# Performance work log

Measured on AMD Instinct MI355X. Metric: run time of the kernel, lower is better.

The kernel has to match this reference:

```python
import jax, jax.numpy as jnp
import numpy as np

B, C, H, W = 4, 256, 64, 64
CI = C // 2
EPS = 1e-5


def setup_inputs() -> dict:
    key = jax.random.key(0)
    ks = jax.random.split(key, 3)
    return {
        "x": jax.random.normal(ks[0], (B, C, H, W), dtype=jnp.float32) * 0.1,
        "g_w": jax.random.normal(ks[1], (CI, C), dtype=jnp.float32) * 0.05,
        "g_b": jnp.zeros((CI,), dtype=jnp.float32),
        "W_w": jax.random.normal(ks[2], (C, CI), dtype=jnp.float32) * 0.05,
        "W_b": jnp.zeros((C,), dtype=jnp.float32),
        "gamma": jnp.ones((C,), dtype=jnp.float32),
        "beta": jnp.zeros((C,), dtype=jnp.float32),
    }


def reference(x, g_w, g_b, W_w, W_b, gamma, beta):
    b, c, h, w = x.shape
    n = h * w
    ci = g_w.shape[0]
    # g: 1x1 conv C -> C/2
    g_x = jnp.einsum('oc,bchw->bohw', g_w, x) + g_b[None, :, None, None]
    g_x = g_x.reshape(b, ci, n).transpose(0, 2, 1)          # [B, N, Ci]
    theta = x.reshape(b, c, n).transpose(0, 2, 1)           # [B, N, C]
    phi = x.reshape(b, c, n)                                # [B, C, N]
    f = jnp.einsum('bnc,bcm->bnm', theta, phi)              # [B, N, N]
    attn = jax.nn.softmax(f, axis=-1)
    y = jnp.einsum('bnm,bmc->bnc', attn, g_x)               # [B, N, Ci]
    y = y.transpose(0, 2, 1).reshape(b, ci, h, w)
    # W: 1x1 conv C/2 -> C, then BatchNorm2d (training-mode batch stats)
    wy = jnp.einsum('oc,bchw->bohw', W_w, y) + W_b[None, :, None, None]
    mean = wy.mean(axis=(0, 2, 3))
    var = wy.var(axis=(0, 2, 3))  # biased, as torch BN uses for normalization
    wy = (wy - mean[None, :, None, None]) * jax.lax.rsqrt(var[None, :, None, None] + EPS)
    wy = wy * gamma[None, :, None, None] + beta[None, :, None, None]
    return wy + x
```

## Files before the change

kernel.cpp:

```cpp
#include <hip/hip_runtime.h>
#include <math.h>

#define B_ 4
#define C_ 256
#define CI_ 128
#define N_ 4096
#define QT_ 128
#define KT_ 64
#define KH_ 2048
#define NITER (KH_ / KT_)
#define KSTRIDE 264
#define VSTRIDE 72
constexpr float EPS_ = 1e-5f;

typedef __attribute__((ext_vector_type(8))) short bfrag;
typedef __attribute__((ext_vector_type(4))) float f4;

__device__ __forceinline__ unsigned short bf16r(float x) {
    unsigned u = __float_as_uint(x);
    u += 0x7FFFu + ((u >> 16) & 1u);
    return (unsigned short)(u >> 16);
}
__device__ __forceinline__ unsigned pack_bf16(float a, float b) {
    unsigned ua = __float_as_uint(a); ua += 0x7FFFu + ((ua >> 16) & 1u);
    unsigned ub = __float_as_uint(b); ub += 0x7FFFu + ((ub >> 16) & 1u);
    return (ua >> 16) | (ub & 0xFFFF0000u);
}

__global__ __launch_bounds__(256) void make_xt(const float* __restrict__ x,
                                               unsigned short* __restrict__ xt,
                                               float* __restrict__ sums) {
    if (blockIdx.x == 0 && blockIdx.y == 0 && blockIdx.z == 0) {
        sums[threadIdx.x] = 0.f;
        sums[threadIdx.x + 256] = 0.f;
    }
    int n  = blockIdx.x * 256 + threadIdx.x;
    int c0 = blockIdx.y * 8;
    int b  = blockIdx.z;
    const float* xb = x + (size_t)b * C_ * N_;
    unsigned short buf[8];
#pragma unroll
    for (int c = 0; c < 8; c++) buf[c] = bf16r(xb[(c0 + c) * N_ + n]);
    uint4 v;
    v.x = buf[0] | ((unsigned)buf[1] << 16);
    v.y = buf[2] | ((unsigned)buf[3] << 16);
    v.z = buf[4] | ((unsigned)buf[5] << 16);
    v.w = buf[6] | ((unsigned)buf[7] << 16);
    *(uint4*)&xt[((size_t)b * N_ + n) * C_ + c0] = v;
}

__global__ __launch_bounds__(256) void gconv(const float* __restrict__ x,
                                             const float* __restrict__ gw,
                                             const float* __restrict__ gb,
                                             unsigned short* __restrict__ gx) {
    int m  = blockIdx.x * 256 + threadIdx.x;
    int o0 = blockIdx.y * 16;
    int b  = blockIdx.z;
    const float* xb = x + (size_t)b * C_ * N_;
    float acc[16];
#pragma unroll
    for (int o = 0; o < 16; o++) acc[o] = gb[o0 + o];
    for (int c0 = 0; c0 < C_; c0 += 8) {
        float xv[8];
#pragma unroll
        for (int j = 0; j < 8; j++) xv[j] = xb[(c0 + j) * N_ + m];
#pragma unroll
        for (int o = 0; o < 16; o++) {
            const float* wr = gw + (size_t)(o0 + o) * C_ + c0;
#pragma unroll
            for (int j = 0; j < 8; j++) acc[o] += wr[j] * xv[j];
        }
    }
#pragma unroll
    for (int o = 0; o < 16; o++)
        gx[((size_t)b * CI_ + o0 + o) * N_ + m] = bf16r(acc[o]);
}

__global__ __launch_bounds__(1024, 4) void attn(const unsigned short* __restrict__ xt,
                                                const unsigned short* __restrict__ gx,
                                                float* __restrict__ Yp,
                                                float* __restrict__ ml) {
    __shared__ __align__(16) unsigned short Ks[2][64 * KSTRIDE];
    __shared__ __align__(16) unsigned short Vs[2][128 * VSTRIDE];
    __shared__ __align__(16) unsigned short Ps[128 * VSTRIDE];

    const int tid  = threadIdx.x;
    const int lane = tid & 63, w = tid >> 6;
    const int wq = w & 7, g = w >> 3;
    const int quad = lane >> 4, ql = lane & 15;
    const int half = blockIdx.x & 1;
    const int b    = (blockIdx.x & 7) >> 1;
    const int qt   = blockIdx.x >> 3;
    const int n0   = qt * QT_;
    const int kbase = half * KH_;
    const unsigned short* xtb = xt + (size_t)b * N_ * C_;
    const unsigned short* gxb = gx + (size_t)b * CI_ * N_;

    bfrag qb[8];
#pragma unroll
    for (int ks = 0; ks < 8; ks++)
        qb[ks] = *(const bfrag*)(xtb + (size_t)(n0 + 16 * wq + ql) * C_ + 32 * ks + quad * 8);

    f4 yacc[8];
    const f4 zero4 = {0.f, 0.f, 0.f, 0.f};
#pragma unroll
    for (int i = 0; i < 8; i++) yacc[i] = zero4;
    float mrun = -INFINITY, lrun = 0.f;

    uint4 kreg[2], vreg[1];
#pragma unroll
    for (int r = 0; r < 2; r++) {
        int idx = r * 1024 + tid;
        kreg[r] = *(const uint4*)(xtb + (size_t)(kbase + (idx >> 5)) * C_ + (idx & 31) * 8);
    }
    vreg[0] = *(const uint4*)(gxb + (size_t)(tid >> 3) * N_ + kbase + (tid & 7) * 8);
#pragma unroll
    for (int r = 0; r < 2; r++) {
        int idx = r * 1024 + tid;
        *(uint4*)&Ks[0][(idx >> 5) * KSTRIDE + (idx & 31) * 8] = kreg[r];
    }
    *(uint4*)&Vs[0][(tid >> 3) * VSTRIDE + (tid & 7) * 8] = vreg[0];
#pragma unroll
    for (int r = 0; r < 2; r++) {
        int idx = r * 1024 + tid;
        kreg[r] = *(const uint4*)(xtb + (size_t)(kbase + KT_ + (idx >> 5)) * C_ + (idx & 31) * 8);
    }
    vreg[0] = *(const uint4*)(gxb + (size_t)(tid >> 3) * N_ + kbase + KT_ + (tid & 7) * 8);
    __syncthreads();

    for (int it = 0; it < NITER; ++it) {
        const int cur = it & 1, nxt = cur ^ 1;

        if (it + 1 < NITER) {
#pragma unroll
            for (int r = 0; r < 2; r++) {
                int idx = r * 1024 + tid;
                *(uint4*)&Ks[nxt][(idx >> 5) * KSTRIDE + (idx & 31) * 8] = kreg[r];
            }
            *(uint4*)&Vs[nxt][(tid >> 3) * VSTRIDE + (tid & 7) * 8] = vreg[0];
        }
        if (it + 2 < NITER) {
            const int t0 = kbase + (it + 2) * KT_;
#pragma unroll
            for (int r = 0; r < 2; r++) {
                int idx = r * 1024 + tid;
                kreg[r] = *(const uint4*)(xtb + (size_t)(t0 + (idx >> 5)) * C_ + (idx & 31) * 8);
            }
            vreg[0] = *(const uint4*)(gxb + (size_t)(tid >> 3) * N_ + t0 + (tid & 7) * 8);
        }

        f4 sacc[2];
        sacc[0] = zero4; sacc[1] = zero4;
#pragma unroll
        for (int ks = 0; ks < 8; ks++) {
            bfrag ka[2];
#pragma unroll
            for (int i = 0; i < 2; i++)
                ka[i] = *(const bfrag*)&Ks[cur][(32 * g + 16 * i + ql) * KSTRIDE + 32 * ks + quad * 8];
#pragma unroll
            for (int i = 0; i < 2; i++)
                sacc[i] = __builtin_amdgcn_mfma_f32_16x16x32_bf16(ka[i], qb[ks], sacc[i], 0, 0, 0);
        }

        float mx = -INFINITY;
#pragma unroll
        for (int i = 0; i < 2; i++)
#pragma unroll
            for (int r = 0; r < 4; r++) mx = fmaxf(mx, sacc[i][r]);
        mx = fmaxf(mx, __shfl_xor(mx, 16, 64));
        mx = fmaxf(mx, __shfl_xor(mx, 32, 64));
        float mn = fmaxf(mrun, mx);
        float alpha = __expf(mrun - mn);
        mrun = mn;
        lrun *= alpha;
        if (__any(alpha != 1.f)) {
#pragma unroll
            for (int i = 0; i < 8; i++) {
                yacc[i][0] *= alpha; yacc[i][1] *= alpha;
                yacc[i][2] *= alpha; yacc[i][3] *= alpha;
            }
        }

        {
            int q = 16 * wq + ql;
            float lsum = 0.f;
#pragma unroll
            for (int i = 0; i < 2; i++) {
                float p0 = __expf(sacc[i][0] - mrun);
                float p1 = __expf(sacc[i][1] - mrun);
                float p2 = __expf(sacc[i][2] - mrun);
                float p3 = __expf(sacc[i][3] - mrun);
                lsum += (p0 + p1) + (p2 + p3);
                int idx = q * VSTRIDE + 32 * g + 16 * i + 4 * quad;
                unsigned long long pv = (unsigned long long)pack_bf16(p0, p1)
                                      | ((unsigned long long)pack_bf16(p2, p3) << 32);
                *(unsigned long long*)&Ps[idx] = pv;
            }
            lrun += lsum;
        }

        {
            bfrag pb, va[8];
            pb = *(const bfrag*)&Ps[(16 * wq + ql) * VSTRIDE + 32 * g + quad * 8];
#pragma unroll
            for (int i = 0; i < 8; i++)
                va[i] = *(const bfrag*)&Vs[cur][(16 * i + ql) * VSTRIDE + 32 * g + quad * 8];
#pragma unroll
            for (int i = 0; i < 8; i++)
                yacc[i] = __builtin_amdgcn_mfma_f32_16x16x32_bf16(va[i], pb, yacc[i], 0, 0, 0);
        }

        __syncthreads();
    }

    lrun += __shfl_xor(lrun, 16, 64);
    lrun += __shfl_xor(lrun, 32, 64);

    float* PsF = (float*)Ps;
    float* Ysc = PsF;
    float* mlb = PsF + 4096;

    const int q = 16 * wq + ql;
    if (quad == 0) {
        mlb[(g * 128 + q) * 2]     = mrun;
        mlb[(g * 128 + q) * 2 + 1] = lrun;
    }
    __syncthreads();
    float m0 = mlb[q * 2],           l0 = mlb[q * 2 + 1];
    float m1 = mlb[(128 + q) * 2],   l1 = mlb[(128 + q) * 2 + 1];
    float mm = fmaxf(m0, m1);
    float e0 = __expf(m0 - mm), e1 = __expf(m1 - mm);
    float lnew = e0 * l0 + e1 * l1;

#pragma unroll
    for (int c = 0; c < 4; c++) {
        if (g == 1) {
#pragma unroll
            for (int i2 = 0; i2 < 2; i2++) {
                int i = 2 * c + i2;
#pragma unroll
                for (int r = 0; r < 4; r++) {
                    int cip = 16 * i2 + 4 * quad + r;
                    Ysc[cip * 128 + q] = e1 * yacc[i][r];
                }
            }
        }
        __syncthreads();
        if (g == 0) {
#pragma unroll
            for (int i2 = 0; i2 < 2; i2++) {
                int i = 2 * c + i2;
#pragma unroll
                for (int r = 0; r < 4; r++) {
                    int ci = 16 * i + 4 * quad + r;
                    float v = e0 * yacc[i][r] + Ysc[(16 * i2 + 4 * quad + r) * 128 + q];
                    Yp[(((size_t)half * 4 + b) * CI_ + ci) * N_ + n0 + q] = v;
                }
            }
        }
        __syncthreads();
    }
    if (g == 0 && quad == 0) {
        ml[(((size_t)half * 4 + b) * N_ + n0 + q) * 2]     = mm;
        ml[(((size_t)half * 4 + b) * N_ + n0 + q) * 2 + 1] = lnew;
    }
}

__global__ __launch_bounds__(256) void merge(const float* __restrict__ Yp,
                                             const float* __restrict__ ml,
                                             float* __restrict__ y) {
    int n4 = blockIdx.x * 256 + threadIdx.x;
    int ci = blockIdx.y;
    int b  = blockIdx.z;
    int n  = n4 * 4;
    float4 a0 = *(const float4*)&ml[((size_t)b * N_ + n) * 2];
    float4 a1 = *(const float4*)&ml[((size_t)b * N_ + n + 2) * 2];
    float4 c0 = *(const float4*)&ml[(((size_t)4 + b) * N_ + n) * 2];
    float4 c1 = *(const float4*)&ml[(((size_t)4 + b) * N_ + n + 2) * 2];
    float m0[4] = {a0.x, a0.z, a1.x, a1.z};
    float l0[4] = {a0.y, a0.w, a1.y, a1.w};
    float m1[4] = {c0.x, c0.z, c1.x, c1.z};
    float l1[4] = {c0.y, c0.w, c1.y, c1.w};
    float w0[4], w1[4];
#pragma unroll
    for (int k = 0; k < 4; k++) {
        float mm = fmaxf(m0[k], m1[k]);
        float e0 = __expf(m0[k] - mm), e1 = __expf(m1[k] - mm);
        float inv = 1.f / (e0 * l0[k] + e1 * l1[k]);
        w0[k] = e0 * inv;
        w1[k] = e1 * inv;
    }
    size_t base = ((size_t)b * CI_ + ci) * N_ + n;
    float4 y0 = *(const float4*)&Yp[base];
    float4 y1 = *(const float4*)&Yp[(size_t)4 * CI_ * N_ + base];
    float4 o;
    o.x = w0[0] * y0.x + w1[0] * y1.x;
    o.y = w0[1] * y0.y + w1[1] * y1.y;
    o.z = w0[2] * y0.z + w1[2] * y1.z;
    o.w = w0[3] * y0.w + w1[3] * y1.w;
    *(float4*)&y[base] = o;
}

__global__ __launch_bounds__(256) void wconv_stats(const float* __restrict__ y,
                                                   const float* __restrict__ Ww,
                                                   const float* __restrict__ Wb,
                                                   float* __restrict__ wy,
                                                   float* __restrict__ sums) {
    int n   = blockIdx.x * 256 + threadIdx.x;
    int co0 = blockIdx.y * 16;
    int b   = blockIdx.z;
    const float* yb = y + (size_t)b * CI_ * N_;
    float acc[16];
#pragma unroll
    for (int o = 0; o < 16; o++) acc[o] = Wb[co0 + o];
    for (int c0 = 0; c0 < CI_; c0 += 8) {
        float yv[8];
#pragma unroll
        for (int j = 0; j < 8; j++) yv[j] = yb[(c0 + j) * N_ + n];
#pragma unroll
        for (int o = 0; o < 16; o++) {
            const float* wr = Ww + (size_t)(co0 + o) * CI_ + c0;
#pragma unroll
            for (int j = 0; j < 8; j++) acc[o] += wr[j] * yv[j];
        }
    }
    float* wyb = wy + (size_t)b * C_ * N_;
#pragma unroll
    for (int o = 0; o < 16; o++) wyb[(co0 + o) * N_ + n] = acc[o];

    __shared__ float wred[32][4];
    int lane = threadIdx.x & 63, wid = threadIdx.x >> 6;
#pragma unroll
    for (int o = 0; o < 16; o++) {
        float s1 = acc[o], s2 = acc[o] * acc[o];
#pragma unroll
        for (int off = 32; off > 0; off >>= 1) {
            s1 += __shfl_down(s1, off, 64);
            s2 += __shfl_down(s2, off, 64);
        }
        if (lane == 0) { wred[o][wid] = s1; wred[16 + o][wid] = s2; }
    }
    __syncthreads();
    if (threadIdx.x < 32) {
        int qq = threadIdx.x;
        float t = wred[qq][0] + wred[qq][1] + wred[qq][2] + wred[qq][3];
        int o = qq & 15;
        if (qq < 16) atomicAdd(&sums[co0 + o], t);
        else         atomicAdd(&sums[256 + co0 + o], t);
    }
}

__global__ __launch_bounds__(256) void bn_finalize(float* __restrict__ wy,
                                                   const float* __restrict__ x,
                                                   const float* __restrict__ sums,
                                                   const float* __restrict__ gamma,
                                                   const float* __restrict__ beta,
                                                   float* __restrict__ out) {
    int n4 = blockIdx.x * 256 + threadIdx.x;
    int co = blockIdx.y;
    int b  = blockIdx.z;
    float cnt  = (float)(B_ * N_);
    float mean = sums[co] / cnt;
    float var  = sums[256 + co] / cnt - mean * mean;
    float sc   = rsqrtf(var + EPS_) * gamma[co];
    float bt   = beta[co];
    size_t idx = ((size_t)b * C_ + co) * N_ + (size_t)n4 * 4;
    float4 wv = *(const float4*)&wy[idx];
    float4 xv = *(const float4*)&x[idx];
    float4 o;
    o.x = (wv.x - mean) * sc + bt + xv.x;
    o.y = (wv.y - mean) * sc + bt + xv.y;
    o.z = (wv.z - mean) * sc + bt + xv.z;
    o.w = (wv.w - mean) * sc + bt + xv.w;
    *(float4*)&out[idx] = o;
}

extern "C" void kernel_launch(void* const* d_in, const int* in_sizes, int n_in,
                              void* d_out, int out_size, void* d_ws, size_t ws_size,
                              hipStream_t stream) {
    const float* x     = (const float*)d_in[0];
    const float* gw    = (const float*)d_in[1];
    const float* gb    = (const float*)d_in[2];
    const float* Ww    = (const float*)d_in[3];
    const float* Wb    = (const float*)d_in[4];
    const float* gamma = (const float*)d_in[5];
    const float* beta  = (const float*)d_in[6];
    float* out = (float*)d_out;
    float* ws  = (float*)d_ws;

    unsigned short* xt  = (unsigned short*)ws;
    unsigned short* gxb = (unsigned short*)(ws + 2097152);
    float* Yp   = ws + 3145728;
    float* ml   = ws + 7340032;
    float* sums = ws + 7405568;
    float* y    = ws;
    float* wy   = out;

    hipLaunchKernelGGL(make_xt, dim3(16, 32, 4), dim3(256), 0, stream, x, xt, sums);
    hipLaunchKernelGGL(gconv, dim3(16, 8, 4), dim3(256), 0, stream, x, gw, gb, gxb);
    hipLaunchKernelGGL(attn, dim3(256), dim3(1024), 0, stream, xt, gxb, Yp, ml);
    hipLaunchKernelGGL(merge, dim3(4, 128, 4), dim3(256), 0, stream, Yp, ml, y);
    hipLaunchKernelGGL(wconv_stats, dim3(16, 16, 4), dim3(256), 0, stream, y, Ww, Wb, wy, sums);
    hipLaunchKernelGGL(bn_finalize, dim3(4, 256, 4), dim3(256), 0, stream, wy, x, sums, gamma, beta, out);
}
```

Measured before the change: 283.5 us.

## Switch attention kernel to 32x32x16 MFMA tiles with 512-thread blocks

Reworks the attention kernel to use 32x32x16 bf16 MFMA instead of 16x16x32, with 8 waves per block (4 query groups by 2 key halves) instead of 16. Each wave now owns a 32-query by 32-key tile, so it issues fewer, larger MFMAs and reuses each LDS fragment load across more arithmetic. Two independent score accumulators are summed to shorten the dependency chain. The cost is higher register pressure per thread (16 Q fragments and four 16-wide accumulators) and fewer waves per block available to hide latency.

```diff
diff --git a/kernel.cpp b/kernel.cpp
--- a/kernel.cpp
+++ b/kernel.cpp
@@ -15,6 +15,7 @@
 
 typedef __attribute__((ext_vector_type(8))) short bfrag;
 typedef __attribute__((ext_vector_type(4))) float f4;
+typedef __attribute__((ext_vector_type(16))) float facc16;
 
 __device__ __forceinline__ unsigned short bf16r(float x) {
     unsigned u = __float_as_uint(x);
@@ -76,18 +77,18 @@
         gx[((size_t)b * CI_ + o0 + o) * N_ + m] = bf16r(acc[o]);
 }
 
-__global__ __launch_bounds__(1024, 4) void attn(const unsigned short* __restrict__ xt,
-                                                const unsigned short* __restrict__ gx,
-                                                float* __restrict__ Yp,
-                                                float* __restrict__ ml) {
+__global__ __launch_bounds__(512, 2) void attn(const unsigned short* __restrict__ xt,
+                                               const unsigned short* __restrict__ gx,
+                                               float* __restrict__ Yp,
+                                               float* __restrict__ ml) {
     __shared__ __align__(16) unsigned short Ks[2][64 * KSTRIDE];
     __shared__ __align__(16) unsigned short Vs[2][128 * VSTRIDE];
     __shared__ __align__(16) unsigned short Ps[128 * VSTRIDE];
 
     const int tid  = threadIdx.x;
     const int lane = tid & 63, w = tid >> 6;
-    const int wq = w & 7, g = w >> 3;
-    const int quad = lane >> 4, ql = lane & 15;
+    const int wq = w & 3, g = w >> 2;
+    const int col = lane & 31, h = lane >> 5;
     const int half = blockIdx.x & 1;
     const int b    = (blockIdx.x & 7) >> 1;
     const int qt   = blockIdx.x >> 3;
@@ -96,36 +97,49 @@
     const unsigned short* xtb = xt + (size_t)b * N_ * C_;
     const unsigned short* gxb = gx + (size_t)b * CI_ * N_;
 
-    bfrag qb[8];
-#pragma unroll
-    for (int ks = 0; ks < 8; ks++)
-        qb[ks] = *(const bfrag*)(xtb + (size_t)(n0 + 16 * wq + ql) * C_ + 32 * ks + quad * 8);
-
-    f4 yacc[8];
-    const f4 zero4 = {0.f, 0.f, 0.f, 0.f};
-#pragma unroll
-    for (int i = 0; i < 8; i++) yacc[i] = zero4;
+    bfrag qb[16];
+#pragma unroll
+    for (int kc = 0; kc < 16; kc++)
+        qb[kc] = *(const bfrag*)(xtb + (size_t)(n0 + 32 * wq + col) * C_ + kc * 16 + h * 8);
+
+    facc16 yacc[4];
+#pragma unroll
+    for (int t = 0; t < 4; t++)
+#pragma unroll
+        for (int r = 0; r < 16; r++) yacc[t][r] = 0.f;
     float mrun = -INFINITY, lrun = 0.f;
 
-    uint4 kreg[2], vreg[1];
+    uint4 kreg[4], vreg[2];
+#pragma unroll
+    for (int r = 0; r < 4; r++) {
+        int idx = r * 512 + tid;
+        kreg[r] = *(const uint4*)(xtb + (size_t)(kbase + (idx >> 5)) * C_ + (idx & 31) * 8);
+    }
 #pragma unroll
     for (int r = 0; r < 2; r++) {
-        int idx = r * 1024 + tid;
-        kreg[r] = *(const uint4*)(xtb + (size_t)(kbase + (idx >> 5)) * C_ + (idx & 31) * 8);
-    }
-    vreg[0] = *(const uint4*)(gxb + (size_t)(tid >> 3) * N_ + kbase + (tid & 7) * 8);
+        int idx = r * 512 + tid;
+        vreg[r] = *(const uint4*)(gxb + (size_t)(idx >> 3) * N_ + kbase + (idx & 7) * 8);
+    }
+#pragma unroll
+    for (int r = 0; r < 4; r++) {
+        int idx = r * 512 + tid;
+        *(uint4*)&Ks[0][(idx >> 5) * KSTRIDE + (idx & 31) * 8] = kreg[r];
+    }
 #pragma unroll
     for (int r = 0; r < 2; r++) {
-        int idx = r * 1024 + tid;
-        *(uint4*)&Ks[0][(idx >> 5) * KSTRIDE + (idx & 31) * 8] = kreg[r];
-    }
-    *(uint4*)&Vs[0][(tid >> 3) * VSTRIDE + (tid & 7) * 8] = vreg[0];
+        int idx = r * 512 + tid;
+        *(uint4*)&Vs[0][(idx >> 3) * VSTRIDE + (idx & 7) * 8] = vreg[r];
+    }
+#pragma unroll
+    for (int r = 0; r < 4; r++) {
+        int idx = r * 512 + tid;
+        kreg[r] = *(const uint4*)(xtb + (size_t)(kbase + KT_ + (idx >> 5)) * C_ + (idx & 31) * 8);
+    }
 #pragma unroll
     for (int r = 0; r < 2; r++) {
-        int idx = r * 1024 + tid;
-        kreg[r] = *(const uint4*)(xtb + (size_t)(kbase + KT_ + (idx >> 5)) * C_ + (idx & 31) * 8);
-    }
-    vreg[0] = *(const uint4*)(gxb + (size_t)(tid >> 3) * N_ + kbase + KT_ + (tid & 7) * 8);
+        int idx = r * 512 + tid;
+        vreg[r] = *(const uint4*)(gxb + (size_t)(idx >> 3) * N_ + kbase + KT_ + (idx & 7) * 8);
+    }
     __syncthreads();
 
     for (int it = 0; it < NITER; ++it) {
@@ -133,41 +147,45 @@
 
         if (it + 1 < NITER) {
 #pragma unroll
+            for (int r = 0; r < 4; r++) {
+                int idx = r * 512 + tid;
+                *(uint4*)&Ks[nxt][(idx >> 5) * KSTRIDE + (idx & 31) * 8] = kreg[r];
+            }
+#pragma unroll
             for (int r = 0; r < 2; r++) {
-                int idx = r * 1024 + tid;
-                *(uint4*)&Ks[nxt][(idx >> 5) * KSTRIDE + (idx & 31) * 8] = kreg[r];
-            }
-            *(uint4*)&Vs[nxt][(tid >> 3) * VSTRIDE + (tid & 7) * 8] = vreg[0];
+                int idx = r * 512 + tid;
+                *(uint4*)&Vs[nxt][(idx >> 3) * VSTRIDE + (idx & 7) * 8] = vreg[r];
+            }
         }
         if (it + 2 < NITER) {
             const int t0 = kbase + (it + 2) * KT_;
 #pragma unroll
+            for (int r = 0; r < 4; r++) {
+                int idx = r * 512 + tid;
+                kreg[r] = *(const uint4*)(xtb + (size_t)(t0 + (idx >> 5)) * C_ + (idx & 31) * 8);
+            }
+#pragma unroll
             for (int r = 0; r < 2; r++) {
-                int idx = r * 1024 + tid;
-                kreg[r] = *(const uint4*)(xtb + (size_t)(t0 + (idx >> 5)) * C_ + (idx & 31) * 8);
-            }
-            vreg[0] = *(const uint4*)(gxb + (size_t)(tid >> 3) * N_ + t0 + (tid & 7) * 8);
-        }
-
-        f4 sacc[2];
-        sacc[0] = zero4; sacc[1] = zero4;
-#pragma unroll
-        for (int ks = 0; ks < 8; ks++) {
-            bfrag ka[2];
-#pragma unroll
-            for (int i = 0; i < 2; i++)
-                ka[i] = *(const bfrag*)&Ks[cur][(32 * g + 16 * i + ql) * KSTRIDE + 32 * ks + quad * 8];
-#pragma unroll
-            for (int i = 0; i < 2; i++)
-                sacc[i] = __builtin_amdgcn_mfma_f32_16x16x32_bf16(ka[i], qb[ks], sacc[i], 0, 0, 0);
-        }
+                int idx = r * 512 + tid;
+                vreg[r] = *(const uint4*)(gxb + (size_t)(idx >> 3) * N_ + t0 + (idx & 7) * 8);
+            }
+        }
+
+        facc16 sa, sb;
+#pragma unroll
+        for (int r = 0; r < 16; r++) { sa[r] = 0.f; sb[r] = 0.f; }
+#pragma unroll
+        for (int kc = 0; kc < 8; kc++) {
+            bfrag ka0 = *(const bfrag*)&Ks[cur][(32 * g + col) * KSTRIDE + (2 * kc) * 16 + h * 8];
+            bfrag ka1 = *(const bfrag*)&Ks[cur][(32 * g + col) * KSTRIDE + (2 * kc + 1) * 16 + h * 8];
+            sa = __builtin_amdgcn_mfma_f32_32x32x16_bf16(ka0, qb[2 * kc], sa, 0, 0, 0);
+            sb = __builtin_amdgcn_mfma_f32_32x32x16_bf16(ka1, qb[2 * kc + 1], sb, 0, 0, 0);
+        }
+        facc16 sacc = sa + sb;
 
         float mx = -INFINITY;
 #pragma unroll
-        for (int i = 0; i < 2; i++)
-#pragma unroll
-            for (int r = 0; r < 4; r++) mx = fmaxf(mx, sacc[i][r]);
-        mx = fmaxf(mx, __shfl_xor(mx, 16, 64));
+        for (int r = 0; r < 16; r++) mx = fmaxf(mx, sacc[r]);
         mx = fmaxf(mx, __shfl_xor(mx, 32, 64));
         float mn = fmaxf(mrun, mx);
         float alpha = __expf(mrun - mn);
@@ -175,53 +193,51 @@
         lrun *= alpha;
         if (__any(alpha != 1.f)) {
 #pragma unroll
-            for (int i = 0; i < 8; i++) {
-                yacc[i][0] *= alpha; yacc[i][1] *= alpha;
-                yacc[i][2] *= alpha; yacc[i][3] *= alpha;
-            }
+            for (int t = 0; t < 4; t++)
+#pragma unroll
+                for (int r = 0; r < 16; r++) yacc[t][r] *= alpha;
         }
 
         {
-            int q = 16 * wq + ql;
+            const int q = 32 * wq + col;
             float lsum = 0.f;
 #pragma unroll
-            for (int i = 0; i < 2; i++) {
-                float p0 = __expf(sacc[i][0] - mrun);
-                float p1 = __expf(sacc[i][1] - mrun);
-                float p2 = __expf(sacc[i][2] - mrun);
-                float p3 = __expf(sacc[i][3] - mrun);
-                lsum += (p0 + p1) + (p2 + p3);
-                int idx = q * VSTRIDE + 32 * g + 16 * i + 4 * quad;
-                unsigned long long pv = (unsigned long long)pack_bf16(p0, p1)
-                                      | ((unsigned long long)pack_bf16(p2, p3) << 32);
-                *(unsigned long long*)&Ps[idx] = pv;
+            for (int r = 0; r < 16; r++) {
+                sacc[r] = __expf(sacc[r] - mrun);
+                lsum += sacc[r];
             }
             lrun += lsum;
-        }
-
-        {
-            bfrag pb, va[8];
-            pb = *(const bfrag*)&Ps[(16 * wq + ql) * VSTRIDE + 32 * g + quad * 8];
-#pragma unroll
-            for (int i = 0; i < 8; i++)
-                va[i] = *(const bfrag*)&Vs[cur][(16 * i + ql) * VSTRIDE + 32 * g + quad * 8];
-#pragma unroll
-            for (int i = 0; i < 8; i++)
-                yacc[i] = __builtin_amdgcn_mfma_f32_16x16x32_bf16(va[i], pb, yacc[i], 0, 0, 0);
+#pragma unroll
+            for (int rq = 0; rq < 4; rq++) {
+                unsigned lo = pack_bf16(sacc[4 * rq + 0], sacc[4 * rq + 1]);
+                unsigned hi = pack_bf16(sacc[4 * rq + 2], sacc[4 * rq + 3]);
+                unsigned long long pv = (unsigned long long)lo
+                                      | ((unsigned long long)hi << 32);
+                *(unsigned long long*)&Ps[q * VSTRIDE + 32 * g + 8 * rq + 4 * h] = pv;
+            }
+        }
+
+#pragma unroll
+        for (int mc = 0; mc < 2; mc++) {
+            bfrag pb = *(const bfrag*)&Ps[(32 * wq + col) * VSTRIDE + 32 * g + mc * 16 + h * 8];
+#pragma unroll
+            for (int ct = 0; ct < 4; ct++) {
+                bfrag va = *(const bfrag*)&Vs[cur][(32 * ct + col) * VSTRIDE + 32 * g + mc * 16 + h * 8];
+                yacc[ct] = __builtin_amdgcn_mfma_f32_32x32x16_bf16(va, pb, yacc[ct], 0, 0, 0);
+            }
         }
 
         __syncthreads();
     }
 
-    lrun += __shfl_xor(lrun, 16, 64);
     lrun += __shfl_xor(lrun, 32, 64);
 
     float* PsF = (float*)Ps;
     float* Ysc = PsF;
     float* mlb = PsF + 4096;
 
-    const int q = 16 * wq + ql;
-    if (quad == 0) {
+    const int q = 32 * wq + col;
+    if (h == 0) {
         mlb[(g * 128 + q) * 2]     = mrun;
         mlb[(g * 128 + q) * 2 + 1] = lrun;
     }
@@ -233,34 +249,26 @@
     float lnew = e0 * l0 + e1 * l1;
 
 #pragma unroll
-    for (int c = 0; c < 4; c++) {
+    for (int ct = 0; ct < 4; ct++) {
         if (g == 1) {
 #pragma unroll
-            for (int i2 = 0; i2 < 2; i2++) {
-                int i = 2 * c + i2;
-#pragma unroll
-                for (int r = 0; r < 4; r++) {
-                    int cip = 16 * i2 + 4 * quad + r;
-                    Ysc[cip * 128 + q] = e1 * yacc[i][r];
-                }
+            for (int r = 0; r < 16; r++) {
+                int cl = (r & 3) + 8 * (r >> 2) + 4 * h;
+                Ysc[cl * 128 + q] = e1 * yacc[ct][r];
             }
         }
         __syncthreads();
         if (g == 0) {
 #pragma unroll
-            for (int i2 = 0; i2 < 2; i2++) {
-                int i = 2 * c + i2;
-#pragma unroll
-                for (int r = 0; r < 4; r++) {
-                    int ci = 16 * i + 4 * quad + r;
-                    float v = e0 * yacc[i][r] + Ysc[(16 * i2 + 4 * quad + r) * 128 + q];
-                    Yp[(((size_t)half * 4 + b) * CI_ + ci) * N_ + n0 + q] = v;
-                }
+            for (int r = 0; r < 16; r++) {
+                int cl = (r & 3) + 8 * (r >> 2) + 4 * h;
+                float v = e0 * yacc[ct][r] + Ysc[cl * 128 + q];
+                Yp[(((size_t)half * 4 + b) * CI_ + 32 * ct + cl) * N_ + n0 + q] = v;
             }
         }
         __syncthreads();
     }
-    if (g == 0 && quad == 0) {
+    if (g == 0 && h == 0) {
         ml[(((size_t)half * 4 + b) * N_ + n0 + q) * 2]     = mm;
         ml[(((size_t)half * 4 + b) * N_ + n0 + q) * 2 + 1] = lnew;
     }
@@ -398,7 +406,7 @@
 
     hipLaunchKernelGGL(make_xt, dim3(16, 32, 4), dim3(256), 0, stream, x, xt, sums);
     hipLaunchKernelGGL(gconv, dim3(16, 8, 4), dim3(256), 0, stream, x, gw, gb, gxb);
-    hipLaunchKernelGGL(attn, dim3(256), dim3(1024), 0, stream, xt, gxb, Yp, ml);
+    hipLaunchKernelGGL(attn, dim3(256), dim3(512), 0, stream, xt, gxb, Yp, ml);
     hipLaunchKernelGGL(merge, dim3(4, 128, 4), dim3(256), 0, stream, Yp, ml, y);
     hipLaunchKernelGGL(wconv_stats, dim3(16, 16, 4), dim3(256), 0, stream, y, Ww, Wb, wy, sums);
     hipLaunchKernelGGL(bn_finalize, dim3(4, 256, 4), dim3(256), 0, stream, wy, x, sums, gamma, beta, out);
```

New measurement: 280.4 us. About the same (-1.1%).

## Software-pipeline PV matmul one tile behind QK, swizzle LDS, lazy rescale

Applied to the files above, without the earlier changes.

Restructures the attention loop so the P·V MFMAs for the previous tile run after the QK^T MFMAs for the current tile. This needs double-buffered P and triple-buffered V in shared memory. Padded LDS strides are replaced with XOR swizzles to avoid bank conflicts without padding. The online-softmax max update becomes lazy: it only rescales when the new max exceeds the running one by more than 8. That removes most rescale exponentials and multiplies, at the cost of a looser numerical bound on intermediate values. Shared memory use grows and the final reduction scratch is moved onto the K buffer.

```diff
diff --git a/kernel.cpp b/kernel.cpp
--- a/kernel.cpp
+++ b/kernel.cpp
@@ -9,8 +9,6 @@
 #define KT_ 64
 #define KH_ 2048
 #define NITER (KH_ / KT_)
-#define KSTRIDE 264
-#define VSTRIDE 72
 constexpr float EPS_ = 1e-5f;
 
 typedef __attribute__((ext_vector_type(8))) short bfrag;
@@ -80,9 +78,9 @@
                                                 const unsigned short* __restrict__ gx,
                                                 float* __restrict__ Yp,
                                                 float* __restrict__ ml) {
-    __shared__ __align__(16) unsigned short Ks[2][64 * KSTRIDE];
-    __shared__ __align__(16) unsigned short Vs[2][128 * VSTRIDE];
-    __shared__ __align__(16) unsigned short Ps[128 * VSTRIDE];
+    __shared__ __align__(16) unsigned short Ks[2][64 * 256];
+    __shared__ __align__(16) unsigned short Vs[3][128 * 64];
+    __shared__ __align__(16) unsigned short Ps[2][128 * 64];
 
     const int tid  = threadIdx.x;
     const int lane = tid & 63, w = tid >> 6;
@@ -105,39 +103,59 @@
     const f4 zero4 = {0.f, 0.f, 0.f, 0.f};
 #pragma unroll
     for (int i = 0; i < 8; i++) yacc[i] = zero4;
-    float mrun = -INFINITY, lrun = 0.f;
-
-    uint4 kreg[2], vreg[1];
+    float mrun = -INFINITY, lrun = 0.f, aprev = 1.f;
+
+    uint4 kreg[2], vreg;
 #pragma unroll
     for (int r = 0; r < 2; r++) {
         int idx = r * 1024 + tid;
         kreg[r] = *(const uint4*)(xtb + (size_t)(kbase + (idx >> 5)) * C_ + (idx & 31) * 8);
     }
-    vreg[0] = *(const uint4*)(gxb + (size_t)(tid >> 3) * N_ + kbase + (tid & 7) * 8);
+    vreg = *(const uint4*)(gxb + (size_t)(tid >> 3) * N_ + kbase + (tid & 7) * 8);
 #pragma unroll
     for (int r = 0; r < 2; r++) {
         int idx = r * 1024 + tid;
-        *(uint4*)&Ks[0][(idx >> 5) * KSTRIDE + (idx & 31) * 8] = kreg[r];
-    }
-    *(uint4*)&Vs[0][(tid >> 3) * VSTRIDE + (tid & 7) * 8] = vreg[0];
+        int row = idx >> 5, gr = idx & 31;
+        *(uint4*)&Ks[0][row * 256 + ((gr ^ (row & 31)) << 3)] = kreg[r];
+    }
+    {
+        int row = tid >> 3, gr = tid & 7;
+        *(uint4*)&Vs[0][row * 64 + ((gr ^ (row & 7)) << 3)] = vreg;
+    }
 #pragma unroll
     for (int r = 0; r < 2; r++) {
         int idx = r * 1024 + tid;
         kreg[r] = *(const uint4*)(xtb + (size_t)(kbase + KT_ + (idx >> 5)) * C_ + (idx & 31) * 8);
     }
-    vreg[0] = *(const uint4*)(gxb + (size_t)(tid >> 3) * N_ + kbase + KT_ + (tid & 7) * 8);
+    vreg = *(const uint4*)(gxb + (size_t)(tid >> 3) * N_ + kbase + KT_ + (tid & 7) * 8);
     __syncthreads();
+
+    int vbw = 1;
 
     for (int it = 0; it < NITER; ++it) {
         const int cur = it & 1, nxt = cur ^ 1;
 
+        f4 sacc[2];
+        sacc[0] = zero4; sacc[1] = zero4;
+#pragma unroll
+        for (int ks = 0; ks < 8; ks++) {
+            bfrag ka0 = *(const bfrag*)&Ks[cur][(32 * g + ql) * 256
+                                               + (((4 * ks + quad) ^ ql) << 3)];
+            bfrag ka1 = *(const bfrag*)&Ks[cur][(32 * g + 16 + ql) * 256
+                                               + (((4 * ks + quad) ^ (16 + ql)) << 3)];
+            sacc[0] = __builtin_amdgcn_mfma_f32_16x16x32_bf16(ka0, qb[ks], sacc[0], 0, 0, 0);
+            sacc[1] = __builtin_amdgcn_mfma_f32_16x16x32_bf16(ka1, qb[ks], sacc[1], 0, 0, 0);
+        }
+
         if (it + 1 < NITER) {
 #pragma unroll
             for (int r = 0; r < 2; r++) {
                 int idx = r * 1024 + tid;
-                *(uint4*)&Ks[nxt][(idx >> 5) * KSTRIDE + (idx & 31) * 8] = kreg[r];
-            }
-            *(uint4*)&Vs[nxt][(tid >> 3) * VSTRIDE + (tid & 7) * 8] = vreg[0];
+                int row = idx >> 5, gr = idx & 31;
+                *(uint4*)&Ks[nxt][row * 256 + ((gr ^ (row & 31)) << 3)] = kreg[r];
+            }
+            int row = tid >> 3, gr = tid & 7;
+            *(uint4*)&Vs[vbw][row * 64 + ((gr ^ (row & 7)) << 3)] = vreg;
         }
         if (it + 2 < NITER) {
             const int t0 = kbase + (it + 2) * KT_;
@@ -146,43 +164,47 @@
                 int idx = r * 1024 + tid;
                 kreg[r] = *(const uint4*)(xtb + (size_t)(t0 + (idx >> 5)) * C_ + (idx & 31) * 8);
             }
-            vreg[0] = *(const uint4*)(gxb + (size_t)(tid >> 3) * N_ + t0 + (tid & 7) * 8);
-        }
-
-        f4 sacc[2];
-        sacc[0] = zero4; sacc[1] = zero4;
-#pragma unroll
-        for (int ks = 0; ks < 8; ks++) {
-            bfrag ka[2];
+            vreg = *(const uint4*)(gxb + (size_t)(tid >> 3) * N_ + t0 + (tid & 7) * 8);
+        }
+
+        if (it > 0) {
+            if (__any(aprev != 1.f)) {
+#pragma unroll
+                for (int i = 0; i < 8; i++) {
+                    yacc[i][0] *= aprev; yacc[i][1] *= aprev;
+                    yacc[i][2] *= aprev; yacc[i][3] *= aprev;
+                }
+            }
+            const int vbr = (vbw == 2) ? 0 : vbw + 1;
+            const int vswz = ((4 * g + quad) ^ (ql & 7)) << 3;
+            bfrag pb = *(const bfrag*)&Ps[nxt][(16 * wq + ql) * 64 + vswz];
+            bfrag va[8];
+#pragma unroll
+            for (int i = 0; i < 8; i++)
+                va[i] = *(const bfrag*)&Vs[vbr][(16 * i + ql) * 64 + vswz];
+#pragma unroll
+            for (int i = 0; i < 8; i++)
+                yacc[i] = __builtin_amdgcn_mfma_f32_16x16x32_bf16(va[i], pb, yacc[i], 0, 0, 0);
+        }
+
+        {
+            float mx = -INFINITY;
 #pragma unroll
             for (int i = 0; i < 2; i++)
-                ka[i] = *(const bfrag*)&Ks[cur][(32 * g + 16 * i + ql) * KSTRIDE + 32 * ks + quad * 8];
-#pragma unroll
-            for (int i = 0; i < 2; i++)
-                sacc[i] = __builtin_amdgcn_mfma_f32_16x16x32_bf16(ka[i], qb[ks], sacc[i], 0, 0, 0);
-        }
-
-        float mx = -INFINITY;
-#pragma unroll
-        for (int i = 0; i < 2; i++)
-#pragma unroll
-            for (int r = 0; r < 4; r++) mx = fmaxf(mx, sacc[i][r]);
-        mx = fmaxf(mx, __shfl_xor(mx, 16, 64));
-        mx = fmaxf(mx, __shfl_xor(mx, 32, 64));
-        float mn = fmaxf(mrun, mx);
-        float alpha = __expf(mrun - mn);
-        mrun = mn;
-        lrun *= alpha;
-        if (__any(alpha != 1.f)) {
-#pragma unroll
-            for (int i = 0; i < 8; i++) {
-                yacc[i][0] *= alpha; yacc[i][1] *= alpha;
-                yacc[i][2] *= alpha; yacc[i][3] *= alpha;
-            }
-        }
-
-        {
-            int q = 16 * wq + ql;
+#pragma unroll
+                for (int r = 0; r < 4; r++) mx = fmaxf(mx, sacc[i][r]);
+            mx = fmaxf(mx, __shfl_xor(mx, 16, 64));
+            mx = fmaxf(mx, __shfl_xor(mx, 32, 64));
+            if (__any(mx > mrun + 8.f)) {
+                float mn = fmaxf(mrun, mx);
+                aprev = __expf(mrun - mn);
+                lrun *= aprev;
+                mrun = mn;
+            } else {
+                aprev = 1.f;
+            }
+
+            const int q = 16 * wq + ql;
             float lsum = 0.f;
 #pragma unroll
             for (int i = 0; i < 2; i++) {
@@ -191,34 +213,45 @@
                 float p2 = __expf(sacc[i][2] - mrun);
                 float p3 = __expf(sacc[i][3] - mrun);
                 lsum += (p0 + p1) + (p2 + p3);
-                int idx = q * VSTRIDE + 32 * g + 16 * i + 4 * quad;
+                int gsw = ((4 * g + 2 * i + (quad >> 1)) ^ (ql & 7)) << 3;
                 unsigned long long pv = (unsigned long long)pack_bf16(p0, p1)
                                       | ((unsigned long long)pack_bf16(p2, p3) << 32);
-                *(unsigned long long*)&Ps[idx] = pv;
+                *(unsigned long long*)&Ps[cur][q * 64 + gsw + 4 * (quad & 1)] = pv;
             }
             lrun += lsum;
         }
 
-        {
-            bfrag pb, va[8];
-            pb = *(const bfrag*)&Ps[(16 * wq + ql) * VSTRIDE + 32 * g + quad * 8];
-#pragma unroll
-            for (int i = 0; i < 8; i++)
-                va[i] = *(const bfrag*)&Vs[cur][(16 * i + ql) * VSTRIDE + 32 * g + quad * 8];
-#pragma unroll
-            for (int i = 0; i < 8; i++)
-                yacc[i] = __builtin_amdgcn_mfma_f32_16x16x32_bf16(va[i], pb, yacc[i], 0, 0, 0);
-        }
-
         __syncthreads();
+        vbw = (vbw == 2) ? 0 : vbw + 1;
+    }
+
+    if (__any(aprev != 1.f)) {
+#pragma unroll
+        for (int i = 0; i < 8; i++) {
+            yacc[i][0] *= aprev; yacc[i][1] *= aprev;
+            yacc[i][2] *= aprev; yacc[i][3] *= aprev;
+        }
+    }
+    {
+        const int fp = (NITER - 1) & 1;
+        const int fv = (NITER - 1) % 3;
+        const int vswz = ((4 * g + quad) ^ (ql & 7)) << 3;
+        bfrag pb = *(const bfrag*)&Ps[fp][(16 * wq + ql) * 64 + vswz];
+        bfrag va[8];
+#pragma unroll
+        for (int i = 0; i < 8; i++)
+            va[i] = *(const bfrag*)&Vs[fv][(16 * i + ql) * 64 + vswz];
+#pragma unroll
+        for (int i = 0; i < 8; i++)
+            yacc[i] = __builtin_amdgcn_mfma_f32_16x16x32_bf16(va[i], pb, yacc[i], 0, 0, 0);
     }
 
     lrun += __shfl_xor(lrun, 16, 64);
     lrun += __shfl_xor(lrun, 32, 64);
 
-    float* PsF = (float*)Ps;
-    float* Ysc = PsF;
-    float* mlb = PsF + 4096;
+    float* KsF = (float*)Ks;
+    float* Ysc = KsF;
+    float* mlb = KsF + 4096;
 
     const int q = 16 * wq + ql;
     if (quad == 0) {
```

Measured after the change: 294.3 us. 1.04x slower.
